# Kernel tuning notes

Hardware: AMD Instinct MI355X
Metric: run time of the kernel (lower is better)

The kernel has to match this reference:

```python
import jax, jax.numpy as jnp
import numpy as np

TAU = 2.0
TH = 1.0


def setup_inputs() -> dict:
    key = jax.random.key(0)
    x = jax.random.normal(key, (32, 512, 2048), dtype=jnp.float32)  # [B, T, D]
    return {"x": x}


def reference(x):
    # Leaky-integrate-and-fire recurrence over time axis T.
    # v_t = v_{t-1} + (x_t - v_{t-1}) / tau
    # s_t = sigmoid(v_t - th)          (surrogate spike, used as forward output here)
    # v_t = v_t * (1 - s_t)            (soft multiplicative reset)
    B, T, D = x.shape
    xt = jnp.swapaxes(x, 0, 1)  # [T, B, D] for scan

    def step(v, x_t):
        v = v + (x_t - v) / TAU
        s = jax.nn.sigmoid(v - TH)
        v = v * (1.0 - s)
        return v, s

    v0 = jnp.zeros((B, D), dtype=x.dtype)
    _, spikes = jax.lax.scan(step, v0, xt)  # spikes: [T, B, D]
    return jnp.swapaxes(spikes, 0, 1)  # [B, T, D]
```

## Files before the change

kernel.cpp:

```cpp
#include <hip/hip_runtime.h>
#include <math.h>


#define TAU_INV 0.5f
#define TH 1.0f

constexpr int BATCH = 32;
constexpr int TT = 512;
constexpr int DD = 2048;
constexpr int U = 16;
constexpr int NB = TT / U;

__global__ __launch_bounds__(256) void lif_kernel(const float* __restrict__ x,
                                                  float* __restrict__ out) {
    int tid = blockIdx.x * blockDim.x + threadIdx.x;
    int b = tid >> 11;
    int d = tid & (DD - 1);
    const float* xp = x + (size_t)b * TT * DD + d;
    float* op = out + (size_t)b * TT * DD + d;

    float buf[2][U];

    #pragma unroll
    for (int i = 0; i < U; ++i)
        buf[0][i] = __builtin_nontemporal_load(xp + (size_t)i * DD);

    float v = 0.0f;
    #pragma unroll 2
    for (int blk = 0; blk < NB; ++blk) {
        const int cur = blk & 1;
        const int nxt = cur ^ 1;

        if (blk + 1 < NB) {
            const float* xn = xp + (size_t)(blk + 1) * U * DD;
            #pragma unroll
            for (int i = 0; i < U; ++i)
                buf[nxt][i] = __builtin_nontemporal_load(xn + (size_t)i * DD);
        }

        float* ob = op + (size_t)blk * U * DD;
        #pragma unroll
        for (int i = 0; i < U; ++i) {
            v = v + (buf[cur][i] - v) * TAU_INV;
            float s = 1.0f / (1.0f + __expf(TH - v));
            __builtin_nontemporal_store(s, ob + (size_t)i * DD);
            v = v * (1.0f - s);
        }
    }
}

extern "C" void kernel_launch(void* const* d_in, const int* in_sizes, int n_in,
                              void* d_out, int out_size, void* d_ws, size_t ws_size,
                              hipStream_t stream) {
    const float* x = (const float*)d_in[0];
    float* out = (float*)d_out;
    const int threads = 256;
    const int total = BATCH * DD;
    const int blocks = (total + threads - 1) / threads;
    lif_kernel<<<blocks, threads, 0, stream>>>(x, out);
}
```

Before: 225.9 us.

## Split time axis into segments with warmup recurrence to raise parallelism

```diff
diff --git a/kernel.cpp b/kernel.cpp
--- a/kernel.cpp
+++ b/kernel.cpp
@@ -8,37 +8,60 @@
 constexpr int BATCH = 32;
 constexpr int TT = 512;
 constexpr int DD = 2048;
-constexpr int U = 16;
-constexpr int NB = TT / U;
+constexpr int S = 8;
+constexpr int SEG = TT / S;
+constexpr int W = 32;
+constexpr int U = 8;
+static_assert(SEG % U == 0 && W % U == 0, "chunking");
 
-__global__ __launch_bounds__(256) void lif_kernel(const float* __restrict__ x,
-                                                  float* __restrict__ out) {
+__global__ __launch_bounds__(256, 8) void lif_kernel(const float* __restrict__ x,
+                                                     float* __restrict__ out) {
     int tid = blockIdx.x * blockDim.x + threadIdx.x;
-    int b = tid >> 11;
     int d = tid & (DD - 1);
+    int rest = tid >> 11;
+    int sg = rest & (S - 1);
+    int b = rest >> 3;
     const float* xp = x + (size_t)b * TT * DD + d;
     float* op = out + (size_t)b * TT * DD + d;
+    const int t0 = sg * SEG;
 
+    float v = 0.0f;
+
+    if (sg != 0) {
+        const float* xw = xp + (size_t)(t0 - W) * DD;
+        #pragma unroll 1
+        for (int c = 0; c < W / U; ++c) {
+            float buf[U];
+            #pragma unroll
+            for (int i = 0; i < U; ++i)
+                buf[i] = xw[(size_t)(c * U + i) * DD];
+            #pragma unroll
+            for (int i = 0; i < U; ++i) {
+                v = v + (buf[i] - v) * TAU_INV;
+                float s = 1.0f / (1.0f + __expf(TH - v));
+                v = v * (1.0f - s);
+            }
+        }
+    }
+
+    const float* xm = xp + (size_t)t0 * DD;
+    float* om = op + (size_t)t0 * DD;
     float buf[2][U];
-
     #pragma unroll
     for (int i = 0; i < U; ++i)
-        buf[0][i] = __builtin_nontemporal_load(xp + (size_t)i * DD);
+        buf[0][i] = xm[(size_t)i * DD];
 
-    float v = 0.0f;
     #pragma unroll 2
-    for (int blk = 0; blk < NB; ++blk) {
-        const int cur = blk & 1;
+    for (int c = 0; c < SEG / U; ++c) {
+        const int cur = c & 1;
         const int nxt = cur ^ 1;
-
-        if (blk + 1 < NB) {
-            const float* xn = xp + (size_t)(blk + 1) * U * DD;
+        if (c + 1 < SEG / U) {
+            const float* xn = xm + (size_t)(c + 1) * U * DD;
             #pragma unroll
             for (int i = 0; i < U; ++i)
-                buf[nxt][i] = __builtin_nontemporal_load(xn + (size_t)i * DD);
+                buf[nxt][i] = xn[(size_t)i * DD];
         }
-
-        float* ob = op + (size_t)blk * U * DD;
+        float* ob = om + (size_t)c * U * DD;
         #pragma unroll
         for (int i = 0; i < U; ++i) {
             v = v + (buf[cur][i] - v) * TAU_INV;
@@ -55,7 +78,7 @@
     const float* x = (const float*)d_in[0];
     float* out = (float*)d_out;
     const int threads = 256;
-    const int total = BATCH * DD;
-    const int blocks = (total + threads - 1) / threads;
+    const int total = BATCH * S * DD;
+    const int blocks = total / threads;
     lif_kernel<<<blocks, threads, 0, stream>>>(x, out);
 }
```

Measured after the change: 242.8 us. 7.5% more time.
